# Kernel optimization log

Hardware: AMD Instinct MI355X
Metric: run time of the kernel (lower is better)

## Reference

```python
import jax, jax.numpy as jnp
from jax import lax
import numpy as np

B, L, D = 16, 512, 256
F, K = 256, 3
M = 2048
EPS = 1e-5


def setup_inputs() -> dict:
    key = jax.random.key(0)
    ks = jax.random.split(key, 12)
    x = jax.random.normal(ks[0], (B, L, D), jnp.float32)
    # integer durations >= 1, sum over L <= 3*512 = 1536 < M, as in training targets
    target = jax.random.randint(ks[1], (B, L), 1, 4)
    s = 0.02
    conv1_w = jax.random.normal(ks[2], (F, D, K), jnp.float32) * s
    conv1_b = jnp.zeros((F,), jnp.float32)
    ln1_g = jnp.ones((F,), jnp.float32)
    ln1_b = jnp.zeros((F,), jnp.float32)
    conv2_w = jax.random.normal(ks[3], (F, F, K), jnp.float32) * s
    conv2_b = jnp.zeros((F,), jnp.float32)
    ln2_g = jnp.ones((F,), jnp.float32)
    ln2_b = jnp.zeros((F,), jnp.float32)
    lin_w = jax.random.normal(ks[4], (F, 1), jnp.float32) * s
    lin_b = jnp.zeros((1,), jnp.float32)
    return dict(x=x, target=target, mel_max_length=M,
                conv1_w=conv1_w, conv1_b=conv1_b, ln1_g=ln1_g, ln1_b=ln1_b,
                conv2_w=conv2_w, conv2_b=conv2_b, ln2_g=ln2_g, ln2_b=ln2_b,
                lin_w=lin_w, lin_b=lin_b)


def _layer_norm(h, g, b):
    mu = jnp.mean(h, axis=-1, keepdims=True)
    var = jnp.mean(jnp.square(h - mu), axis=-1, keepdims=True)
    return (h - mu) * lax.rsqrt(var + EPS) * g + b


def _conv1d(h_bld, w, b):
    # h: (B, L, C_in), w: (C_out, C_in, K) -> (B, L, C_out), SAME padding
    pad = (w.shape[-1] - 1) // 2
    h = jnp.transpose(h_bld, (0, 2, 1))  # (B, C, L)
    h = lax.conv_general_dilated(h, w, (1,), [(pad, pad)],
                                 dimension_numbers=('NCH', 'OIH', 'NCH'))
    return jnp.transpose(h + b[None, :, None], (0, 2, 1))


def _duration_predictor(x, conv1_w, conv1_b, ln1_g, ln1_b,
                        conv2_w, conv2_b, ln2_g, ln2_b, lin_w, lin_b):
    # FastSpeech duration predictor (eval mode: dropout = identity)
    h = jax.nn.relu(_layer_norm(_conv1d(x, conv1_w, conv1_b), ln1_g, ln1_b))
    h = jax.nn.relu(_layer_norm(_conv1d(h, conv2_w, conv2_b), ln2_g, ln2_b))
    return jax.nn.relu(h @ lin_w + lin_b)[..., 0]  # (B, L)


def _length_regulate(x, dur, mel_max_length):
    # alignment[b,m,l] = 1 iff cs[l-1] <= m < cs[l]  (exactly the scatter+diff trick
    # of create_alignment, padded to mel_max_length as in the original F.pad)
    cs = jnp.cumsum(dur, axis=1)              # (B, L) inclusive cumsum
    prev = cs - dur                           # exclusive cumsum
    m = jnp.arange(mel_max_length)[None, :, None]  # (1, M, 1)
    align = ((m >= prev[:, None, :]) & (m < cs[:, None, :])).astype(x.dtype)  # (B,M,L)
    return jnp.einsum('bml,bld->bmd', align, x)


def reference(x, target, mel_max_length, conv1_w, conv1_b, ln1_g, ln1_b,
              conv2_w, conv2_b, ln2_g, ln2_b, lin_w, lin_b):
    dup = _duration_predictor(x, conv1_w, conv1_b, ln1_g, ln1_b,
                              conv2_w, conv2_b, ln2_g, ln2_b, lin_w, lin_b)
    output = _length_regulate(x, target, mel_max_length)
    return (output, dup)
```

## Files before the change

### kernel.cpp

```cpp
#include <hip/hip_runtime.h>
#include <hip/hip_bf16.h>

#define Bn 16
#define Ln 512
#define Cn 256
#define Fn 256
#define Kn 3
#define Mn 2048

#define NKSTEP 24
#define MT 32
#define XS_PS 264
#define NCONVBLK 256
#define NGATH_HALF 2048

typedef __attribute__((ext_vector_type(8))) short short8;
typedef __attribute__((ext_vector_type(4))) float f32x4;

static __device__ __forceinline__ unsigned short f2bf(float f) {
    unsigned int u = __float_as_uint(f);
    return (unsigned short)((u + 0x7fff + ((u >> 16) & 1)) >> 16);
}

static __device__ __forceinline__ void pack_one(const float* __restrict__ w,
                                                unsigned short* __restrict__ bp,
                                                int i) {
    int j    = i & 7;
    int lane = (i >> 3) & 63;
    int nt   = (i >> 9) & 15;
    int s    = i >> 13;
    int kap = s * 32 + ((lane >> 4) * 8) + j;
    int k = kap >> 8;
    int d = kap & 255;
    int f = nt * 16 + (lane & 15);
    bp[i] = f2bf(w[(f * Cn + d) * Kn + k]);
}

__global__ __launch_bounds__(512) void pack_scan(
    const float* __restrict__ w1, const float* __restrict__ w2,
    unsigned short* __restrict__ bp1, unsigned short* __restrict__ bp2,
    const int* __restrict__ target, int* __restrict__ map)
{
    __shared__ int ss[Ln];
    const int blk = blockIdx.x;
    const int t = threadIdx.x;
    if (blk < 768) {
        int i = blk * 512 + t;
        const float* w = w1;
        unsigned short* bp = bp1;
        if (i >= Fn * Cn * Kn) { i -= Fn * Cn * Kn; w = w2; bp = bp2; }
        pack_one(w, bp, i);
        return;
    }
    int b = blk - 768;
    int v = target[b * Ln + t];
    ss[t] = v;
    __syncthreads();
    for (int off = 1; off < Ln; off <<= 1) {
        int add = (t >= off) ? ss[t - off] : 0;
        __syncthreads();
        ss[t] += add;
        __syncthreads();
    }
    int cs    = ss[t];
    int prev  = cs - v;
    int total = ss[Ln - 1];
    for (int m = prev; m < cs; ++m) map[b * Mn + m] = t;
    for (int m = total + t; m < Mn; m += Ln) map[b * Mn + m] = -1;
}

template <bool IS_F32_IN, bool DO_LINEAR, bool WITH_AUX>
__global__ __launch_bounds__(512) void conv_mfma(
    const void* __restrict__ in_,
    const unsigned short* __restrict__ bp,
    const float* __restrict__ bias,
    const float* __restrict__ gamma,
    const float* __restrict__ beta,
    const float* __restrict__ lw,
    const float* __restrict__ lb,
    unsigned short* __restrict__ hout,
    float* __restrict__ dup,
    const float* __restrict__ gx,
    const int* __restrict__ gmap,
    float* __restrict__ gout,
    int gofs)
{
    __shared__ __align__(16) unsigned short xs[(MT + 2) * XS_PS];
    __shared__ float2 red[MT][8];
    __shared__ float  red2[MT][8];

    const int t = threadIdx.x;

    if (WITH_AUX && blockIdx.x >= NCONVBLK) {
        int e4 = (blockIdx.x - NCONVBLK) * 512 + t + gofs;
        int d4 = e4 & 63;
        int bm = e4 >> 6;
        int b  = bm >> 11;
        int l  = gmap[bm];
        float4 val = make_float4(0.f, 0.f, 0.f, 0.f);
        if (l >= 0) val = *((const float4*)(gx + (size_t)(b * Ln + l) * Cn) + d4);
        ((float4*)gout)[e4] = val;
        return;
    }

    const int b  = blockIdx.x >> 4;
    const int l0 = (blockIdx.x & 15) * MT;

    if (IS_F32_IN) {
        const float* in = (const float*)in_;
        for (int idx = t; idx < (MT + 2) * 64; idx += 512) {
            int row = idx >> 6;
            int c4  = (idx & 63) * 4;
            int l = l0 + row - 1;
            float4 v = make_float4(0.f, 0.f, 0.f, 0.f);
            if (l >= 0 && l < Ln) v = *(const float4*)&in[((size_t)b * Ln + l) * Cn + c4];
            unsigned int lo = (unsigned int)f2bf(v.x) | ((unsigned int)f2bf(v.y) << 16);
            unsigned int hi = (unsigned int)f2bf(v.z) | ((unsigned int)f2bf(v.w) << 16);
            *(uint2*)&xs[row * XS_PS + c4] = make_uint2(lo, hi);
        }
    } else {
        const unsigned short* in = (const unsigned short*)in_;
        for (int idx = t; idx < (MT + 2) * 32; idx += 512) {
            int row = idx >> 5;
            int c8  = (idx & 31) * 8;
            int l = l0 + row - 1;
            uint4 v = make_uint4(0u, 0u, 0u, 0u);
            if (l >= 0 && l < Ln) v = *(const uint4*)&in[((size_t)b * Ln + l) * Cn + c8];
            *(uint4*)&xs[row * XS_PS + c8] = v;
        }
    }
    __syncthreads();

    const int lane = t & 63;
    const int wv   = t >> 6;
    const int mrow = lane & 15;
    const int q    = lane >> 4;

    f32x4 acc00 = {}, acc01 = {}, acc10 = {}, acc11 = {};
    short8 a0_0, a1_0, b0_0, b1_0;
    short8 a0_1, a1_1, b0_1, b1_1;

#define LOADB(B0, B1, s_) { \
    const unsigned short* p_ = bp + (size_t)((((s_) * 16) + wv * 2) * 64 + lane) * 8; \
    B0 = *(const short8*)p_; \
    B1 = *(const short8*)(p_ + 512); }
#define LOADA(A0, A1, s_) { \
    const int k_ = (s_) >> 3; \
    const int dc_ = ((s_) & 7) * 32 + q * 8; \
    A0 = *(const short8*)&xs[(mrow + k_) * XS_PS + dc_]; \
    A1 = *(const short8*)&xs[(16 + mrow + k_) * XS_PS + dc_]; }
#define DOMFMA(A0, A1, B0, B1) { \
    acc00 = __builtin_amdgcn_mfma_f32_16x16x32_bf16(A0, B0, acc00, 0, 0, 0); \
    acc01 = __builtin_amdgcn_mfma_f32_16x16x32_bf16(A0, B1, acc01, 0, 0, 0); \
    acc10 = __builtin_amdgcn_mfma_f32_16x16x32_bf16(A1, B0, acc10, 0, 0, 0); \
    acc11 = __builtin_amdgcn_mfma_f32_16x16x32_bf16(A1, B1, acc11, 0, 0, 0); }

    LOADB(b0_0, b1_0, 0) LOADA(a0_0, a1_0, 0)
    LOADB(b0_1, b1_1, 1) LOADA(a0_1, a1_1, 1)

    #pragma unroll
    for (int s = 0; s < NKSTEP; s += 2) {
        DOMFMA(a0_0, a1_0, b0_0, b1_0)
        if (s + 2 < NKSTEP) { LOADB(b0_0, b1_0, s + 2) LOADA(a0_0, a1_0, s + 2) }
        DOMFMA(a0_1, a1_1, b0_1, b1_1)
        if (s + 3 < NKSTEP) { LOADB(b0_1, b1_1, s + 3) LOADA(a0_1, a1_1, s + 3) }
    }
#undef LOADB
#undef LOADA
#undef DOMFMA

    const int c0 = wv * 32 + mrow;
    const int c1 = c0 + 16;
    float bias0 = bias[c0], bias1 = bias[c1];
    float g0 = gamma[c0], g1g = gamma[c1];
    float be0 = beta[c0], be1 = beta[c1];
    float lw0 = 0.f, lw1 = 0.f;
    if (DO_LINEAR) { lw0 = lw[c0]; lw1 = lw[c1]; }

    #pragma unroll
    for (int r = 0; r < 4; ++r) {
        acc00[r] += bias0; acc01[r] += bias1;
        acc10[r] += bias0; acc11[r] += bias1;
    }

    #pragma unroll
    for (int mt = 0; mt < 2; ++mt)
        #pragma unroll
        for (int r = 0; r < 4; ++r) {
            float v0 = mt ? acc10[r] : acc00[r];
            float v1 = mt ? acc11[r] : acc01[r];
            float s  = v0 + v1;
            float sq = v0 * v0 + v1 * v1;
            #pragma unroll
            for (int off = 1; off <= 8; off <<= 1) {
                s  += __shfl_xor(s,  off, 64);
                sq += __shfl_xor(sq, off, 64);
            }
            if (mrow == 0) red[mt * 16 + q * 4 + r][wv] = make_float2(s, sq);
        }
    __syncthreads();

    float muv[2][4], rsv[2][4];
    #pragma unroll
    for (int mt = 0; mt < 2; ++mt)
        #pragma unroll
        for (int r = 0; r < 4; ++r) {
            int row = mt * 16 + q * 4 + r;
            float s = 0.f, sq = 0.f;
            #pragma unroll
            for (int w = 0; w < 8; ++w) {
                float2 p = red[row][w];
                s += p.x; sq += p.y;
            }
            float mu  = s * (1.f / 256.f);
            float var = sq * (1.f / 256.f) - mu * mu;
            muv[mt][r] = mu;
            rsv[mt][r] = rsqrtf(var + 1e-5f);
        }

    if (!DO_LINEAR) {
        #pragma unroll
        for (int mt = 0; mt < 2; ++mt)
            #pragma unroll
            for (int r = 0; r < 4; ++r) {
                float v0 = mt ? acc10[r] : acc00[r];
                float v1 = mt ? acc11[r] : acc01[r];
                int l = l0 + mt * 16 + q * 4 + r;
                size_t base = ((size_t)b * Ln + l) * Fn;
                float o0 = fmaxf((v0 - muv[mt][r]) * rsv[mt][r] * g0  + be0, 0.f);
                float o1 = fmaxf((v1 - muv[mt][r]) * rsv[mt][r] * g1g + be1, 0.f);
                hout[base + c0] = f2bf(o0);
                hout[base + c1] = f2bf(o1);
            }
    } else {
        #pragma unroll
        for (int mt = 0; mt < 2; ++mt)
            #pragma unroll
            for (int r = 0; r < 4; ++r) {
                float v0 = mt ? acc10[r] : acc00[r];
                float v1 = mt ? acc11[r] : acc01[r];
                float o0 = fmaxf((v0 - muv[mt][r]) * rsv[mt][r] * g0  + be0, 0.f);
                float o1 = fmaxf((v1 - muv[mt][r]) * rsv[mt][r] * g1g + be1, 0.f);
                float dot = o0 * lw0 + o1 * lw1;
                #pragma unroll
                for (int off = 1; off <= 8; off <<= 1)
                    dot += __shfl_xor(dot, off, 64);
                if (mrow == 0) red2[mt * 16 + q * 4 + r][wv] = dot;
            }
        __syncthreads();
        if (t < MT) {
            float d = 0.f;
            #pragma unroll
            for (int w = 0; w < 8; ++w) d += red2[t][w];
            dup[b * Ln + l0 + t] = fmaxf(d + lb[0], 0.f);
        }
    }
}

extern "C" void kernel_launch(void* const* d_in, const int* in_sizes, int n_in,
                              void* d_out, int out_size, void* d_ws, size_t ws_size,
                              hipStream_t stream) {
    const float* x    = (const float*)d_in[0];
    const int*   targ = (const int*)d_in[1];
    const float* c1w = (const float*)d_in[3];
    const float* c1b = (const float*)d_in[4];
    const float* g1  = (const float*)d_in[5];
    const float* be1 = (const float*)d_in[6];
    const float* c2w = (const float*)d_in[7];
    const float* c2b = (const float*)d_in[8];
    const float* g2  = (const float*)d_in[9];
    const float* be2 = (const float*)d_in[10];
    const float* lw  = (const float*)d_in[11];
    const float* lb  = (const float*)d_in[12];

    float* out     = (float*)d_out;
    float* out_dup = out + (size_t)Bn * Mn * Cn;

    char* ws = (char*)d_ws;
    unsigned short* bp1 = (unsigned short*)ws;
    unsigned short* bp2 = (unsigned short*)(ws + 393216);
    unsigned short* h1  = (unsigned short*)(ws + 2 * 393216);
    int*            map = (int*)(ws + 2 * 393216 + 4194304);

    pack_scan<<<784, 512, 0, stream>>>(c1w, c2w, bp1, bp2, targ, map);

    conv_mfma<true, false, true><<<NCONVBLK + NGATH_HALF, 512, 0, stream>>>(
        (const void*)x, bp1, c1b, g1, be1, nullptr, nullptr, h1, nullptr,
        x, map, out, 0);

    conv_mfma<false, true, true><<<NCONVBLK + NGATH_HALF, 512, 0, stream>>>(
        (const void*)h1, bp2, c2b, g2, be2, lw, lb, nullptr, out_dup,
        x, map, out, NGATH_HALF * 512);
}
```

Measured before the change: 122.0 us.

## Fuse pack, scan, both convs and gather into one persistent kernel with grid barriers

Replaces three launches with a single 256-block kernel. Each block packs part of the weights, converts its x tile and, for the first 16 blocks, builds the duration map, then everything waits on an atomic grid barrier. Conv1 output stays in LDS, and only the boundary rows are exchanged between neighbouring blocks through a small halo buffer, which removes the full h1 round trip through global memory. The output gather is placed between the barrier arrive and wait so it overlaps with that wait. The risks are spin-barrier cost, a memset launch, the requirement that all 256 blocks be co-resident, and the gather now running on only 256 blocks instead of thousands.

```diff
diff --git a/kernel.cpp b/kernel.cpp
--- a/kernel.cpp
+++ b/kernel.cpp
@@ -7,12 +7,10 @@
 #define Fn 256
 #define Kn 3
 #define Mn 2048
-
 #define NKSTEP 24
 #define MT 32
 #define XS_PS 264
-#define NCONVBLK 256
-#define NGATH_HALF 2048
+#define NBLK 256
 
 typedef __attribute__((ext_vector_type(8))) short short8;
 typedef __attribute__((ext_vector_type(4))) float f32x4;
@@ -36,225 +34,246 @@
     bp[i] = f2bf(w[(f * Cn + d) * Kn + k]);
 }
 
-__global__ __launch_bounds__(512) void pack_scan(
-    const float* __restrict__ w1, const float* __restrict__ w2,
+__global__ __launch_bounds__(512) void mega(
+    const float* __restrict__ x,
+    const int* __restrict__ targ,
+    const float* __restrict__ w1, const float* __restrict__ cb1,
+    const float* __restrict__ g1, const float* __restrict__ be1,
+    const float* __restrict__ w2, const float* __restrict__ cb2,
+    const float* __restrict__ g2, const float* __restrict__ be2,
+    const float* __restrict__ lw, const float* __restrict__ lb,
     unsigned short* __restrict__ bp1, unsigned short* __restrict__ bp2,
-    const int* __restrict__ target, int* __restrict__ map)
+    int* __restrict__ map,
+    unsigned short* __restrict__ halo,
+    int* __restrict__ syncc,
+    float* __restrict__ out,
+    float* __restrict__ dup)
 {
+    __shared__ __align__(16) unsigned short xs1[34 * XS_PS];
+    __shared__ __align__(16) unsigned short xs2[34 * XS_PS];
+    __shared__ float2 red[MT][8];
+    __shared__ float  red2f[MT][8];
     __shared__ int ss[Ln];
-    const int blk = blockIdx.x;
-    const int t = threadIdx.x;
-    if (blk < 768) {
-        int i = blk * 512 + t;
-        const float* w = w1;
-        unsigned short* bp = bp1;
-        if (i >= Fn * Cn * Kn) { i -= Fn * Cn * Kn; w = w2; bp = bp2; }
-        pack_one(w, bp, i);
-        return;
-    }
-    int b = blk - 768;
-    int v = target[b * Ln + t];
-    ss[t] = v;
-    __syncthreads();
-    for (int off = 1; off < Ln; off <<= 1) {
-        int add = (t >= off) ? ss[t - off] : 0;
-        __syncthreads();
-        ss[t] += add;
-        __syncthreads();
-    }
-    int cs    = ss[t];
-    int prev  = cs - v;
-    int total = ss[Ln - 1];
-    for (int m = prev; m < cs; ++m) map[b * Mn + m] = t;
-    for (int m = total + t; m < Mn; m += Ln) map[b * Mn + m] = -1;
-}
-
-template <bool IS_F32_IN, bool DO_LINEAR, bool WITH_AUX>
-__global__ __launch_bounds__(512) void conv_mfma(
-    const void* __restrict__ in_,
-    const unsigned short* __restrict__ bp,
-    const float* __restrict__ bias,
-    const float* __restrict__ gamma,
-    const float* __restrict__ beta,
-    const float* __restrict__ lw,
-    const float* __restrict__ lb,
-    unsigned short* __restrict__ hout,
-    float* __restrict__ dup,
-    const float* __restrict__ gx,
-    const int* __restrict__ gmap,
-    float* __restrict__ gout,
-    int gofs)
-{
-    __shared__ __align__(16) unsigned short xs[(MT + 2) * XS_PS];
-    __shared__ float2 red[MT][8];
-    __shared__ float  red2[MT][8];
-
-    const int t = threadIdx.x;
-
-    if (WITH_AUX && blockIdx.x >= NCONVBLK) {
-        int e4 = (blockIdx.x - NCONVBLK) * 512 + t + gofs;
-        int d4 = e4 & 63;
-        int bm = e4 >> 6;
-        int b  = bm >> 11;
-        int l  = gmap[bm];
-        float4 val = make_float4(0.f, 0.f, 0.f, 0.f);
-        if (l >= 0) val = *((const float4*)(gx + (size_t)(b * Ln + l) * Cn) + d4);
-        ((float4*)gout)[e4] = val;
-        return;
-    }
-
-    const int b  = blockIdx.x >> 4;
-    const int l0 = (blockIdx.x & 15) * MT;
-
-    if (IS_F32_IN) {
-        const float* in = (const float*)in_;
-        for (int idx = t; idx < (MT + 2) * 64; idx += 512) {
-            int row = idx >> 6;
-            int c4  = (idx & 63) * 4;
-            int l = l0 + row - 1;
-            float4 v = make_float4(0.f, 0.f, 0.f, 0.f);
-            if (l >= 0 && l < Ln) v = *(const float4*)&in[((size_t)b * Ln + l) * Cn + c4];
-            unsigned int lo = (unsigned int)f2bf(v.x) | ((unsigned int)f2bf(v.y) << 16);
-            unsigned int hi = (unsigned int)f2bf(v.z) | ((unsigned int)f2bf(v.w) << 16);
-            *(uint2*)&xs[row * XS_PS + c4] = make_uint2(lo, hi);
-        }
-    } else {
-        const unsigned short* in = (const unsigned short*)in_;
-        for (int idx = t; idx < (MT + 2) * 32; idx += 512) {
-            int row = idx >> 5;
-            int c8  = (idx & 31) * 8;
-            int l = l0 + row - 1;
-            uint4 v = make_uint4(0u, 0u, 0u, 0u);
-            if (l >= 0 && l < Ln) v = *(const uint4*)&in[((size_t)b * Ln + l) * Cn + c8];
-            *(uint4*)&xs[row * XS_PS + c8] = v;
-        }
-    }
-    __syncthreads();
-
+
+    const int t    = threadIdx.x;
+    const int blk  = blockIdx.x;
+    const int b    = blk >> 4;
+    const int tile = blk & 15;
+    const int l0   = tile * MT;
     const int lane = t & 63;
     const int wv   = t >> 6;
     const int mrow = lane & 15;
     const int q    = lane >> 4;
-
-    f32x4 acc00 = {}, acc01 = {}, acc10 = {}, acc11 = {};
-    short8 a0_0, a1_0, b0_0, b1_0;
-    short8 a0_1, a1_1, b0_1, b1_1;
-
-#define LOADB(B0, B1, s_) { \
-    const unsigned short* p_ = bp + (size_t)((((s_) * 16) + wv * 2) * 64 + lane) * 8; \
+    const int c0   = wv * 32 + mrow;
+    const int c1   = c0 + 16;
+
+    for (int idx = t; idx < 34 * 64; idx += 512) {
+        int row = idx >> 6;
+        int c4  = (idx & 63) * 4;
+        int l = l0 + row - 1;
+        float4 v = make_float4(0.f, 0.f, 0.f, 0.f);
+        if (l >= 0 && l < Ln) v = *(const float4*)&x[((size_t)b * Ln + l) * Cn + c4];
+        unsigned int lo = (unsigned int)f2bf(v.x) | ((unsigned int)f2bf(v.y) << 16);
+        unsigned int hi = (unsigned int)f2bf(v.z) | ((unsigned int)f2bf(v.w) << 16);
+        *(uint2*)&xs1[row * XS_PS + c4] = make_uint2(lo, hi);
+    }
+    #pragma unroll
+    for (int j = 0; j < 3; ++j) {
+        int i = blk * 1536 + j * 512 + t;
+        if (i < Fn * Cn * Kn) pack_one(w1, bp1, i);
+        else                  pack_one(w2, bp2, i - Fn * Cn * Kn);
+    }
+    if (blk < Bn) {
+        int v = targ[blk * Ln + t];
+        ss[t] = v;
+        __syncthreads();
+        for (int off = 1; off < Ln; off <<= 1) {
+            int add = (t >= off) ? ss[t - off] : 0;
+            __syncthreads();
+            ss[t] += add;
+            __syncthreads();
+        }
+        int cs    = ss[t];
+        int prev  = cs - v;
+        int total = ss[Ln - 1];
+        for (int m = prev; m < cs; ++m) map[blk * Mn + m] = t;
+        for (int m = total + t; m < Mn; m += Ln) map[blk * Mn + m] = -1;
+    }
+
+    __syncthreads();
+    if (t == 0) {
+        __threadfence();
+        __hip_atomic_fetch_add(syncc, 1, __ATOMIC_ACQ_REL, __HIP_MEMORY_SCOPE_AGENT);
+        while (__hip_atomic_load(syncc, __ATOMIC_ACQUIRE, __HIP_MEMORY_SCOPE_AGENT) < NBLK)
+            __builtin_amdgcn_s_sleep(2);
+        __threadfence();
+    }
+    __syncthreads();
+
+#define LOADB(B0, B1, BP, s_) { \
+    const unsigned short* p_ = (BP) + (size_t)((((s_) * 16) + wv * 2) * 64 + lane) * 8; \
     B0 = *(const short8*)p_; \
     B1 = *(const short8*)(p_ + 512); }
-#define LOADA(A0, A1, s_) { \
+#define LOADA(A0, A1, XS, s_) { \
     const int k_ = (s_) >> 3; \
     const int dc_ = ((s_) & 7) * 32 + q * 8; \
-    A0 = *(const short8*)&xs[(mrow + k_) * XS_PS + dc_]; \
-    A1 = *(const short8*)&xs[(16 + mrow + k_) * XS_PS + dc_]; }
+    A0 = *(const short8*)&(XS)[(mrow + k_) * XS_PS + dc_]; \
+    A1 = *(const short8*)&(XS)[(16 + mrow + k_) * XS_PS + dc_]; }
 #define DOMFMA(A0, A1, B0, B1) { \
     acc00 = __builtin_amdgcn_mfma_f32_16x16x32_bf16(A0, B0, acc00, 0, 0, 0); \
     acc01 = __builtin_amdgcn_mfma_f32_16x16x32_bf16(A0, B1, acc01, 0, 0, 0); \
     acc10 = __builtin_amdgcn_mfma_f32_16x16x32_bf16(A1, B0, acc10, 0, 0, 0); \
     acc11 = __builtin_amdgcn_mfma_f32_16x16x32_bf16(A1, B1, acc11, 0, 0, 0); }
-
-    LOADB(b0_0, b1_0, 0) LOADA(a0_0, a1_0, 0)
-    LOADB(b0_1, b1_1, 1) LOADA(a0_1, a1_1, 1)
-
-    #pragma unroll
-    for (int s = 0; s < NKSTEP; s += 2) {
-        DOMFMA(a0_0, a1_0, b0_0, b1_0)
-        if (s + 2 < NKSTEP) { LOADB(b0_0, b1_0, s + 2) LOADA(a0_0, a1_0, s + 2) }
-        DOMFMA(a0_1, a1_1, b0_1, b1_1)
-        if (s + 3 < NKSTEP) { LOADB(b0_1, b1_1, s + 3) LOADA(a0_1, a1_1, s + 3) }
-    }
-#undef LOADB
-#undef LOADA
-#undef DOMFMA
-
-    const int c0 = wv * 32 + mrow;
-    const int c1 = c0 + 16;
-    float bias0 = bias[c0], bias1 = bias[c1];
-    float g0 = gamma[c0], g1g = gamma[c1];
-    float be0 = beta[c0], be1 = beta[c1];
-    float lw0 = 0.f, lw1 = 0.f;
-    if (DO_LINEAR) { lw0 = lw[c0]; lw1 = lw[c1]; }
-
-    #pragma unroll
-    for (int r = 0; r < 4; ++r) {
-        acc00[r] += bias0; acc01[r] += bias1;
-        acc10[r] += bias0; acc11[r] += bias1;
-    }
-
-    #pragma unroll
-    for (int mt = 0; mt < 2; ++mt)
+#define KLOOP(XS, BP) { \
+    short8 a0_0, a1_0, b0_0, b1_0, a0_1, a1_1, b0_1, b1_1; \
+    LOADB(b0_0, b1_0, BP, 0) LOADA(a0_0, a1_0, XS, 0) \
+    LOADB(b0_1, b1_1, BP, 1) LOADA(a0_1, a1_1, XS, 1) \
+    _Pragma("unroll") \
+    for (int s = 0; s < NKSTEP; s += 2) { \
+        DOMFMA(a0_0, a1_0, b0_0, b1_0) \
+        if (s + 2 < NKSTEP) { LOADB(b0_0, b1_0, BP, s + 2) LOADA(a0_0, a1_0, XS, s + 2) } \
+        DOMFMA(a0_1, a1_1, b0_1, b1_1) \
+        if (s + 3 < NKSTEP) { LOADB(b0_1, b1_1, BP, s + 3) LOADA(a0_1, a1_1, XS, s + 3) } \
+    } }
+#define LNSTATS(MU, RS) { \
+    _Pragma("unroll") \
+    for (int mt = 0; mt < 2; ++mt) \
+        _Pragma("unroll") \
+        for (int r = 0; r < 4; ++r) { \
+            float v0 = mt ? acc10[r] : acc00[r]; \
+            float v1 = mt ? acc11[r] : acc01[r]; \
+            float s_ = v0 + v1; \
+            float sq_ = v0 * v0 + v1 * v1; \
+            _Pragma("unroll") \
+            for (int off = 1; off <= 8; off <<= 1) { \
+                s_  += __shfl_xor(s_,  off, 64); \
+                sq_ += __shfl_xor(sq_, off, 64); \
+            } \
+            if (mrow == 0) red[mt * 16 + q * 4 + r][wv] = make_float2(s_, sq_); \
+        } \
+    __syncthreads(); \
+    _Pragma("unroll") \
+    for (int mt = 0; mt < 2; ++mt) \
+        _Pragma("unroll") \
+        for (int r = 0; r < 4; ++r) { \
+            int row_ = mt * 16 + q * 4 + r; \
+            float s_ = 0.f, sq_ = 0.f; \
+            _Pragma("unroll") \
+            for (int w_ = 0; w_ < 8; ++w_) { float2 p_ = red[row_][w_]; s_ += p_.x; sq_ += p_.y; } \
+            float mu_ = s_ * (1.f / 256.f); \
+            float var_ = sq_ * (1.f / 256.f) - mu_ * mu_; \
+            MU[mt][r] = mu_; \
+            RS[mt][r] = rsqrtf(var_ + 1e-5f); \
+        } }
+
+    {
+        f32x4 acc00 = {}, acc01 = {}, acc10 = {}, acc11 = {};
+        KLOOP(xs1, bp1)
+        float bias0 = cb1[c0], bias1 = cb1[c1];
+        float ga0 = g1[c0], ga1 = g1[c1];
+        float bb0 = be1[c0], bb1 = be1[c1];
         #pragma unroll
         for (int r = 0; r < 4; ++r) {
-            float v0 = mt ? acc10[r] : acc00[r];
-            float v1 = mt ? acc11[r] : acc01[r];
-            float s  = v0 + v1;
-            float sq = v0 * v0 + v1 * v1;
-            #pragma unroll
-            for (int off = 1; off <= 8; off <<= 1) {
-                s  += __shfl_xor(s,  off, 64);
-                sq += __shfl_xor(sq, off, 64);
-            }
-            if (mrow == 0) red[mt * 16 + q * 4 + r][wv] = make_float2(s, sq);
-        }
-    __syncthreads();
-
-    float muv[2][4], rsv[2][4];
-    #pragma unroll
-    for (int mt = 0; mt < 2; ++mt)
-        #pragma unroll
-        for (int r = 0; r < 4; ++r) {
-            int row = mt * 16 + q * 4 + r;
-            float s = 0.f, sq = 0.f;
-            #pragma unroll
-            for (int w = 0; w < 8; ++w) {
-                float2 p = red[row][w];
-                s += p.x; sq += p.y;
-            }
-            float mu  = s * (1.f / 256.f);
-            float var = sq * (1.f / 256.f) - mu * mu;
-            muv[mt][r] = mu;
-            rsv[mt][r] = rsqrtf(var + 1e-5f);
-        }
-
-    if (!DO_LINEAR) {
+            acc00[r] += bias0; acc01[r] += bias1;
+            acc10[r] += bias0; acc11[r] += bias1;
+        }
+        float muv[2][4], rsv[2][4];
+        LNSTATS(muv, rsv)
         #pragma unroll
         for (int mt = 0; mt < 2; ++mt)
             #pragma unroll
             for (int r = 0; r < 4; ++r) {
                 float v0 = mt ? acc10[r] : acc00[r];
                 float v1 = mt ? acc11[r] : acc01[r];
-                int l = l0 + mt * 16 + q * 4 + r;
-                size_t base = ((size_t)b * Ln + l) * Fn;
-                float o0 = fmaxf((v0 - muv[mt][r]) * rsv[mt][r] * g0  + be0, 0.f);
-                float o1 = fmaxf((v1 - muv[mt][r]) * rsv[mt][r] * g1g + be1, 0.f);
-                hout[base + c0] = f2bf(o0);
-                hout[base + c1] = f2bf(o1);
+                int rl = mt * 16 + q * 4 + r;
+                unsigned short o0 = f2bf(fmaxf((v0 - muv[mt][r]) * rsv[mt][r] * ga0 + bb0, 0.f));
+                unsigned short o1 = f2bf(fmaxf((v1 - muv[mt][r]) * rsv[mt][r] * ga1 + bb1, 0.f));
+                xs2[(rl + 1) * XS_PS + c0] = o0;
+                xs2[(rl + 1) * XS_PS + c1] = o1;
+                if (rl == 0)  { halo[(blk * 2 + 0) * 256 + c0] = o0; halo[(blk * 2 + 0) * 256 + c1] = o1; }
+                if (rl == 31) { halo[(blk * 2 + 1) * 256 + c0] = o0; halo[(blk * 2 + 1) * 256 + c1] = o1; }
             }
+    }
+
+    __syncthreads();
+    if (t == 0) {
+        __threadfence();
+        __hip_atomic_fetch_add(syncc, 1, __ATOMIC_ACQ_REL, __HIP_MEMORY_SCOPE_AGENT);
+    }
+    {
+        int d4 = t & 15;
+        float4 z = make_float4(0.f, 0.f, 0.f, 0.f);
+        #pragma unroll
+        for (int g = 0; g < 4; ++g) {
+            int bm = blk * 128 + g * 32 + (t >> 4);
+            int gb = bm >> 11;
+            int l  = map[bm];
+            const float4* src = (const float4*)(x + ((size_t)gb * Ln + (l >= 0 ? l : 0)) * Cn) + d4;
+            float4* dst = (float4*)out + (size_t)bm * 64 + d4;
+            #pragma unroll
+            for (int j = 0; j < 4; ++j)
+                dst[j * 16] = (l >= 0) ? src[j * 16] : z;
+        }
+    }
+    if (t == 0) {
+        while (__hip_atomic_load(syncc, __ATOMIC_ACQUIRE, __HIP_MEMORY_SCOPE_AGENT) < 2 * NBLK)
+            __builtin_amdgcn_s_sleep(2);
+        __threadfence();
+    }
+    __syncthreads();
+
+    if (t < 256) {
+        unsigned short hv = 0;
+        if (tile > 0) hv = halo[((blk - 1) * 2 + 1) * 256 + t];
+        xs2[t] = hv;
     } else {
+        int c = t - 256;
+        unsigned short hv = 0;
+        if (tile < 15) hv = halo[((blk + 1) * 2 + 0) * 256 + c];
+        xs2[33 * XS_PS + c] = hv;
+    }
+    __syncthreads();
+    {
+        f32x4 acc00 = {}, acc01 = {}, acc10 = {}, acc11 = {};
+        KLOOP(xs2, bp2)
+        float bias0 = cb2[c0], bias1 = cb2[c1];
+        float ga0 = g2[c0], ga1 = g2[c1];
+        float bb0 = be2[c0], bb1 = be2[c1];
+        float lw0 = lw[c0], lw1 = lw[c1];
+        #pragma unroll
+        for (int r = 0; r < 4; ++r) {
+            acc00[r] += bias0; acc01[r] += bias1;
+            acc10[r] += bias0; acc11[r] += bias1;
+        }
+        float muv[2][4], rsv[2][4];
+        LNSTATS(muv, rsv)
         #pragma unroll
         for (int mt = 0; mt < 2; ++mt)
             #pragma unroll
             for (int r = 0; r < 4; ++r) {
                 float v0 = mt ? acc10[r] : acc00[r];
                 float v1 = mt ? acc11[r] : acc01[r];
-                float o0 = fmaxf((v0 - muv[mt][r]) * rsv[mt][r] * g0  + be0, 0.f);
-                float o1 = fmaxf((v1 - muv[mt][r]) * rsv[mt][r] * g1g + be1, 0.f);
+                float o0 = fmaxf((v0 - muv[mt][r]) * rsv[mt][r] * ga0 + bb0, 0.f);
+                float o1 = fmaxf((v1 - muv[mt][r]) * rsv[mt][r] * ga1 + bb1, 0.f);
                 float dot = o0 * lw0 + o1 * lw1;
                 #pragma unroll
                 for (int off = 1; off <= 8; off <<= 1)
                     dot += __shfl_xor(dot, off, 64);
-                if (mrow == 0) red2[mt * 16 + q * 4 + r][wv] = dot;
+                if (mrow == 0) red2f[mt * 16 + q * 4 + r][wv] = dot;
             }
         __syncthreads();
         if (t < MT) {
             float d = 0.f;
             #pragma unroll
-            for (int w = 0; w < 8; ++w) d += red2[t][w];
+            for (int w = 0; w < 8; ++w) d += red2f[t][w];
             dup[b * Ln + l0 + t] = fmaxf(d + lb[0], 0.f);
         }
     }
+#undef LOADB
+#undef LOADA
+#undef DOMFMA
+#undef KLOOP
+#undef LNSTATS
 }
 
 extern "C" void kernel_launch(void* const* d_in, const int* in_sizes, int n_in,
@@ -277,18 +296,14 @@
     float* out_dup = out + (size_t)Bn * Mn * Cn;
 
     char* ws = (char*)d_ws;
-    unsigned short* bp1 = (unsigned short*)ws;
-    unsigned short* bp2 = (unsigned short*)(ws + 393216);
-    unsigned short* h1  = (unsigned short*)(ws + 2 * 393216);
-    int*            map = (int*)(ws + 2 * 393216 + 4194304);
-
-    pack_scan<<<784, 512, 0, stream>>>(c1w, c2w, bp1, bp2, targ, map);
-
-    conv_mfma<true, false, true><<<NCONVBLK + NGATH_HALF, 512, 0, stream>>>(
-        (const void*)x, bp1, c1b, g1, be1, nullptr, nullptr, h1, nullptr,
-        x, map, out, 0);
-
-    conv_mfma<false, true, true><<<NCONVBLK + NGATH_HALF, 512, 0, stream>>>(
-        (const void*)h1, bp2, c2b, g2, be2, lw, lb, nullptr, out_dup,
-        x, map, out, NGATH_HALF * 512);
+    unsigned short* bp1  = (unsigned short*)ws;
+    unsigned short* bp2  = (unsigned short*)(ws + 393216);
+    int*            map  = (int*)(ws + 786432);
+    unsigned short* halo = (unsigned short*)(ws + 917504);
+    int*            sy   = (int*)(ws + 1179648);
+
+    hipMemsetAsync(sy, 0, 64, stream);
+    mega<<<NBLK, 512, 0, stream>>>(x, targ, c1w, c1b, g1, be1,
+                                   c2w, c2b, g2, be2, lw, lb,
+                                   bp1, bp2, map, halo, sy, out, out_dup);
 }
```

Result: slower. 166.6 us (+36.6%).
